# Kernel tuning notes

Hardware: AMD Instinct MI355X
Metric: run time of the kernel (lower is better)

## Reference

```python
import jax, jax.numpy as jnp
import numpy as np

N, M, K = 262144, 65536, 32
C_IN, C_OUT = 64, 128
BN_EPS = 1e-5


def setup_inputs() -> dict:
    key = jax.random.key(0)
    ks = jax.random.split(key, 6)
    p = jax.random.normal(ks[0], (N, 3), jnp.float32)
    x = jax.random.normal(ks[1], (N, C_IN), jnp.float32)
    o = jnp.array([N], jnp.int32)  # single-cloud batch offsets
    idx = jnp.sort(jax.random.randint(ks[2], (M,), 0, N))  # sampled point indices (FPS stand-in)
    knn_idx = jax.random.randint(ks[3], (M, K), 0, N)      # neighbor indices (ball-query/knn stand-in)
    # learned params: Linear(C_IN+3 -> C_OUT) + BatchNorm1d(C_OUT)
    W = jax.random.normal(ks[4], (C_IN + 3, C_OUT), jnp.float32) / np.sqrt(C_IN + 3).astype(np.float32)
    b = jnp.zeros((C_OUT,), jnp.float32)
    gamma = jnp.ones((C_OUT,), jnp.float32)
    beta = jnp.zeros((C_OUT,), jnp.float32)
    return dict(p=p, x=x, o=o, idx=idx, knn_idx=knn_idx, W=W, b=b, gamma=gamma, beta=beta)


def reference(p, x, o, idx, knn_idx, W, b, gamma, beta):
    # sampler: n_p = p[idx]
    n_p = p[idx]  # [M, 3]
    # pooling with with_xyz=True: gather K neighbors, concat relative xyz, max-pool over K
    rel = p[knn_idx] - n_p[:, None, :]                      # [M, K, 3]
    grouped = jnp.concatenate([rel, x[knn_idx]], axis=-1)   # [M, K, 3+C_IN]
    pooled = grouped.max(axis=1)                            # [M, 3+C_IN]
    # convs: Linear -> BatchNorm1d (training-mode batch stats) -> ReLU
    h = pooled @ W + b                                      # [M, C_OUT]
    mean = h.mean(axis=0)
    var = h.var(axis=0)
    h = (h - mean) * jax.lax.rsqrt(var + BN_EPS) * gamma + beta
    x_out = jnp.maximum(h, 0.0)
    n_o = jnp.array([idx.shape[0]], jnp.int32)
    return (n_p, x_out, n_o)
```

## Files before the change

kernel.cpp:

```cpp
#include <hip/hip_runtime.h>
#include <hip/hip_fp16.h>
#include <math.h>

#define K_NB   32
#define C_IN   64
#define C_OUT  128
#define KP     96
#define TILE   128
#define BN_EPS 1e-5f

typedef _Float16 f16x8 __attribute__((ext_vector_type(8)));
typedef float    f32x4 __attribute__((ext_vector_type(4)));
typedef float    f32x2 __attribute__((ext_vector_type(2)));

__device__ __forceinline__ unsigned pk(float a, float b) {
    __half2 h = __floats2half2_rn(a, b);
    return *reinterpret_cast<unsigned*>(&h);
}

__device__ __forceinline__ unsigned pkmax(unsigned a, unsigned b) {
    unsigned d;
    asm volatile("v_pk_max_f16 %0, %1, %2" : "=v"(d) : "v"(a), "v"(b));
    return d;
}

using pkrtz_t = decltype(__builtin_amdgcn_cvt_pkrtz(0.f, 0.f));
__device__ __forceinline__ unsigned h2u(pkrtz_t v) {
    union { pkrtz_t h; unsigned u; } c; c.h = v; return c.u;
}

__device__ __forceinline__ void fp8x4_to_h2x2(unsigned d, unsigned& lo, unsigned& hi) {
    f32x2 a = __builtin_amdgcn_cvt_pk_f32_fp8((int)d, false);
    f32x2 b = __builtin_amdgcn_cvt_pk_f32_fp8((int)d, true);
    lo = h2u(__builtin_amdgcn_cvt_pkrtz(a.x, a.y));
    hi = h2u(__builtin_amdgcn_cvt_pkrtz(b.x, b.y));
}

__global__ __launch_bounds__(256) void sa_zero(float* __restrict__ g, int n)
{
    for (int i = threadIdx.x; i < n; i += 256) g[i] = 0.f;
}

__global__ __launch_bounds__(256) void sa_cvt(
    const float4* __restrict__ x4, uint4* __restrict__ xq, int n16,
    float* __restrict__ gsum, int ng)
{
    if (blockIdx.x == 0)
        for (int i = threadIdx.x; i < ng; i += 256) gsum[i] = 0.f;
    for (int i = blockIdx.x * blockDim.x + threadIdx.x; i < n16;
         i += gridDim.x * blockDim.x) {
        float4 v0 = x4[4*i+0], v1 = x4[4*i+1], v2 = x4[4*i+2], v3 = x4[4*i+3];
        int w0 = 0, w1 = 0, w2 = 0, w3 = 0;
        w0 = __builtin_amdgcn_cvt_pk_fp8_f32(v0.x, v0.y, w0, false);
        w0 = __builtin_amdgcn_cvt_pk_fp8_f32(v0.z, v0.w, w0, true);
        w1 = __builtin_amdgcn_cvt_pk_fp8_f32(v1.x, v1.y, w1, false);
        w1 = __builtin_amdgcn_cvt_pk_fp8_f32(v1.z, v1.w, w1, true);
        w2 = __builtin_amdgcn_cvt_pk_fp8_f32(v2.x, v2.y, w2, false);
        w2 = __builtin_amdgcn_cvt_pk_fp8_f32(v2.z, v2.w, w2, true);
        w3 = __builtin_amdgcn_cvt_pk_fp8_f32(v3.x, v3.y, w3, false);
        w3 = __builtin_amdgcn_cvt_pk_fp8_f32(v3.z, v3.w, w3, true);
        xq[i] = make_uint4((unsigned)w0, (unsigned)w1, (unsigned)w2, (unsigned)w3);
    }
}

__global__ __launch_bounds__(256) void sa_pool_h(
    const float* __restrict__ p, const uint2* __restrict__ xq2,
    const int* __restrict__ idx, const int* __restrict__ knn,
    float* __restrict__ np_out, float* __restrict__ hbuf)
{
    const int lane = threadIdx.x & 63;
    const int wid  = threadIdx.x >> 6;
    const int m0   = blockIdx.x * 8 + wid * 2;
    const int half = lane >> 5;
    const int m    = m0 + half;

    const int kidx = knn[m0 * K_NB + lane];

    const int sub = lane & 7;
    const int g   = lane >> 3;
    uint2 u[8];
    #pragma unroll
    for (int i = 0; i < 4; ++i) {
        const int nbA = __shfl(kidx, i * 8 + g);
        u[i] = xq2[(size_t)nbA * 8 + sub];
    }
    #pragma unroll
    for (int i = 0; i < 4; ++i) {
        const int nbB = __shfl(kidx, 32 + i * 8 + g);
        u[4 + i] = xq2[(size_t)nbB * 8 + sub];
    }

    unsigned mx0 = 0xFC00FC00u, mx1 = 0xFC00FC00u, mx2 = 0xFC00FC00u, mx3 = 0xFC00FC00u;
    unsigned my0 = 0xFC00FC00u, my1 = 0xFC00FC00u, my2 = 0xFC00FC00u, my3 = 0xFC00FC00u;
    #pragma unroll
    for (int i = 0; i < 4; ++i) {
        unsigned h01, h23, h45, h67;
        fp8x4_to_h2x2(u[i].x, h01, h23);
        fp8x4_to_h2x2(u[i].y, h45, h67);
        mx0 = pkmax(mx0, h01); mx1 = pkmax(mx1, h23);
        mx2 = pkmax(mx2, h45); mx3 = pkmax(mx3, h67);
    }
    #pragma unroll
    for (int i = 0; i < 4; ++i) {
        unsigned h01, h23, h45, h67;
        fp8x4_to_h2x2(u[4 + i].x, h01, h23);
        fp8x4_to_h2x2(u[4 + i].y, h45, h67);
        my0 = pkmax(my0, h01); my1 = pkmax(my1, h23);
        my2 = pkmax(my2, h45); my3 = pkmax(my3, h67);
    }
    #pragma unroll
    for (int off = 8; off <= 32; off <<= 1) {
        mx0 = pkmax(mx0, (unsigned)__shfl_xor((int)mx0, off));
        mx1 = pkmax(mx1, (unsigned)__shfl_xor((int)mx1, off));
        mx2 = pkmax(mx2, (unsigned)__shfl_xor((int)mx2, off));
        mx3 = pkmax(mx3, (unsigned)__shfl_xor((int)mx3, off));
        my0 = pkmax(my0, (unsigned)__shfl_xor((int)my0, off));
        my1 = pkmax(my1, (unsigned)__shfl_xor((int)my1, off));
        my2 = pkmax(my2, (unsigned)__shfl_xor((int)my2, off));
        my3 = pkmax(my3, (unsigned)__shfl_xor((int)my3, off));
    }

    const float* pp = p + (size_t)kidx * 3;
    float px = pp[0], py = pp[1], pz = pp[2];
    #pragma unroll
    for (int off = 16; off >= 1; off >>= 1) {
        px = fmaxf(px, __shfl_xor(px, off));
        py = fmaxf(py, __shfl_xor(py, off));
        pz = fmaxf(pz, __shfl_xor(pz, off));
    }

    const int s = idx[m];
    const float npx = p[(size_t)s*3+0];
    const float npy = p[(size_t)s*3+1];
    const float npz = p[(size_t)s*3+2];
    if (lane < 3)                    np_out[(size_t)m0*3 + lane] = (lane == 0) ? npx : (lane == 1 ? npy : npz);
    else if (lane >= 32 && lane < 35) np_out[(size_t)(m0+1)*3 + (lane-32)] = (lane == 32) ? npx : (lane == 33 ? npy : npz);

    const float rx = px - npx, ry = py - npy, rz = pz - npz;

    const int t0 = m0 >> 7,       rl0 = m0 & (TILE - 1);
    const int t1 = (m0+1) >> 7,   rl1 = (m0+1) & (TILE - 1);
    __half* rowh0 = (__half*)(hbuf + (size_t)t0 * TILE * C_OUT) + rl0 * KP;
    __half* rowh1 = (__half*)(hbuf + (size_t)t1 * TILE * C_OUT) + rl1 * KP;

    if (lane < 8) {
        *(uint4*)(rowh0 + lane * 8) = make_uint4(mx0, mx1, mx2, mx3);
    } else if (lane < 16) {
        *(uint4*)(rowh1 + (lane - 8) * 8) = make_uint4(my0, my1, my2, my3);
    } else if (lane == 16) {
        *(uint4*)(rowh0 + 64) = make_uint4(pk(rx, ry), pk(rz, 0.f), 0u, 0u);
    } else if (lane >= 17 && lane < 20) {
        *(uint4*)(rowh0 + 64 + (lane - 16) * 8) = make_uint4(0u, 0u, 0u, 0u);
    } else if (lane == 48) {
        *(uint4*)(rowh1 + 64) = make_uint4(pk(rx, ry), pk(rz, 0.f), 0u, 0u);
    } else if (lane >= 49 && lane < 52) {
        *(uint4*)(rowh1 + 64 + (lane - 48) * 8) = make_uint4(0u, 0u, 0u, 0u);
    }
}

__global__ __launch_bounds__(256) void sa_pool_f(
    const float* __restrict__ p, const float* __restrict__ x,
    const int* __restrict__ idx, const int* __restrict__ knn,
    float* __restrict__ np_out, float* __restrict__ hbuf)
{
    const int lane = threadIdx.x & 63;
    const int m    = blockIdx.x * 4 + (threadIdx.x >> 6);
    int kidx = 0;
    if (lane < K_NB) kidx = knn[m * K_NB + lane];
    float xmax = -INFINITY;
    #pragma unroll
    for (int k = 0; k < K_NB; ++k) {
        int nb = __shfl(kidx, k);
        xmax = fmaxf(xmax, x[(size_t)nb * C_IN + lane]);
    }
    float px = -INFINITY, py = -INFINITY, pz = -INFINITY;
    if (lane < K_NB) {
        const float* pp = p + (size_t)kidx * 3;
        px = pp[0]; py = pp[1]; pz = pp[2];
    }
    #pragma unroll
    for (int off = 32; off >= 1; off >>= 1) {
        px = fmaxf(px, __shfl_xor(px, off));
        py = fmaxf(py, __shfl_xor(py, off));
        pz = fmaxf(pz, __shfl_xor(pz, off));
    }
    const int s = idx[m];
    const float npx = p[(size_t)s*3], npy = p[(size_t)s*3+1], npz = p[(size_t)s*3+2];
    if (lane < 3) np_out[(size_t)m*3 + lane] = (lane == 0) ? npx : (lane == 1 ? npy : npz);

    const int tile = m >> 7, rl = m & (TILE - 1);
    __half* rowh = (__half*)(hbuf + (size_t)tile * TILE * C_OUT) + rl * KP;
    if (lane < 8) {
        float v[8];
        #pragma unroll
        for (int j = 0; j < 8; ++j) v[j] = __shfl(xmax, lane * 8 + j);
        *(uint4*)(rowh + lane * 8) =
            make_uint4(pk(v[0],v[1]), pk(v[2],v[3]), pk(v[4],v[5]), pk(v[6],v[7]));
    } else if (lane == 8) {
        *(uint4*)(rowh + 64) = make_uint4(pk(px-npx, py-npy), pk(pz-npz, 0.f), 0u, 0u);
    } else if (lane < 12) {
        *(uint4*)(rowh + 64 + (lane - 8) * 8) = make_uint4(0u, 0u, 0u, 0u);
    }
}

__global__ __launch_bounds__(256) void sa_gemm_mfma(
    const float* __restrict__ W, const float* __restrict__ bias,
    float* __restrict__ h, float* __restrict__ gsum, unsigned rep_mask)
{
    __shared__ __half Wt[C_OUT][128];
    __shared__ float reds[16][C_OUT];
    __shared__ float redq[16][C_OUT];

    const int t    = threadIdx.x;
    const int wave = t >> 6, lane = t & 63;
    const int l15  = lane & 15, lg = lane >> 4;
    const int m0   = blockIdx.x * TILE;

    for (int e = t; e < C_OUT * KP; e += 256) {
        const int c = e & 127, kk = e >> 7;
        float w = 0.f;
        if (kk < C_IN)          w = W[(size_t)(3 + kk) * C_OUT + c];
        else if (kk < C_IN + 3) w = W[(size_t)(kk - C_IN) * C_OUT + c];
        Wt[c][(((kk >> 3) ^ (c & 7)) << 3) | (kk & 7)] = __float2half(w);
    }

    const __half* tb = (const __half*)(h + (size_t)blockIdx.x * TILE * C_OUT);
    f16x8 A[2][3];
    #pragma unroll
    for (int rt = 0; rt < 2; ++rt) {
        const int rl = wave * 32 + rt * 16 + l15;
        #pragma unroll
        for (int ks = 0; ks < 3; ++ks)
            A[rt][ks] = *(const f16x8*)(tb + (size_t)rl * KP + ks * 32 + lg * 8);
    }
    __syncthreads();

    f32x4 acc[2][8];
    #pragma unroll
    for (int ct = 0; ct < 8; ++ct) {
        const float bc = bias[ct * 16 + l15];
        acc[0][ct] = (f32x4){bc, bc, bc, bc};
        acc[1][ct] = (f32x4){bc, bc, bc, bc};
    }
    #pragma unroll
    for (int ks = 0; ks < 3; ++ks) {
        #pragma unroll
        for (int ct = 0; ct < 8; ++ct) {
            const int c  = ct * 16 + l15;
            const int kc = ks * 4 + lg;
            const f16x8 wf = *(const f16x8*)&Wt[c][((kc ^ (c & 7)) << 3)];
            acc[0][ct] = __builtin_amdgcn_mfma_f32_16x16x32_f16(A[0][ks], wf, acc[0][ct], 0, 0, 0);
            acc[1][ct] = __builtin_amdgcn_mfma_f32_16x16x32_f16(A[1][ks], wf, acc[1][ct], 0, 0, 0);
        }
    }

    float s8[8], q8[8];
    #pragma unroll
    for (int ct = 0; ct < 8; ++ct) { s8[ct] = 0.f; q8[ct] = 0.f; }
    #pragma unroll
    for (int rt = 0; rt < 2; ++rt) {
        #pragma unroll
        for (int ct = 0; ct < 8; ++ct) {
            const int col = ct * 16 + l15;
            #pragma unroll
            for (int r = 0; r < 4; ++r) {
                const int row = m0 + wave * 32 + rt * 16 + lg * 4 + r;
                const float v = acc[rt][ct][r];
                h[(size_t)row * C_OUT + col] = v;
                s8[ct] += v;
                q8[ct]  = fmaf(v, v, q8[ct]);
            }
        }
    }
    #pragma unroll
    for (int ct = 0; ct < 8; ++ct) {
        reds[wave * 4 + lg][ct * 16 + l15] = s8[ct];
        redq[wave * 4 + lg][ct * 16 + l15] = q8[ct];
    }
    __syncthreads();
    if (t < C_OUT) {
        float ss = 0.f, qq = 0.f;
        #pragma unroll
        for (int i = 0; i < 16; ++i) { ss += reds[i][t]; qq += redq[i][t]; }
        float* g = gsum + (size_t)(blockIdx.x & rep_mask) * 2 * C_OUT;
        atomicAdd(&g[t],         ss);
        atomicAdd(&g[C_OUT + t], qq);
    }
}

__global__ __launch_bounds__(256) void sa_bnrelu_fin(
    float* __restrict__ h, const float* __restrict__ gsum,
    const float* __restrict__ gamma, const float* __restrict__ beta,
    float* __restrict__ no_out, int M, int rep)
{
    __shared__ float sc[C_OUT], sh[C_OUT];
    const int t = threadIdx.x;
    if (t < C_OUT) {
        float s = 0.f, s2 = 0.f;
        for (int r = 0; r < rep; ++r) {
            s  += gsum[(size_t)r * 2 * C_OUT + t];
            s2 += gsum[(size_t)r * 2 * C_OUT + C_OUT + t];
        }
        const float inv_m = 1.0f / (float)M;
        const float mean = s * inv_m;
        const float var  = fmaf(-mean, mean, s2 * inv_m);
        const float scv  = gamma[t] * rsqrtf(var + BN_EPS);
        sc[t] = scv;
        sh[t] = fmaf(-mean, scv, beta[t]);
    }
    if (blockIdx.x == 0 && t == 0) no_out[0] = (float)M;
    __syncthreads();

    const size_t total4 = (size_t)M * C_OUT / 4;
    float4* h4 = (float4*)h;
    for (size_t i = (size_t)blockIdx.x * blockDim.x + t;
         i < total4; i += (size_t)gridDim.x * blockDim.x) {
        float4 v = h4[i];
        const int c = (int)((i * 4) & (C_OUT - 1));
        v.x = fmaxf(fmaf(v.x, sc[c+0], sh[c+0]), 0.f);
        v.y = fmaxf(fmaf(v.y, sc[c+1], sh[c+1]), 0.f);
        v.z = fmaxf(fmaf(v.z, sc[c+2], sh[c+2]), 0.f);
        v.w = fmaxf(fmaf(v.w, sc[c+3], sh[c+3]), 0.f);
        h4[i] = v;
    }
}

extern "C" void kernel_launch(void* const* d_in, const int* in_sizes, int n_in,
                              void* d_out, int out_size, void* d_ws, size_t ws_size,
                              hipStream_t stream)
{
    const float* p     = (const float*)d_in[0];
    const float* x     = (const float*)d_in[1];
    const int*   idx   = (const int*)d_in[3];
    const int*   knn   = (const int*)d_in[4];
    const float* W     = (const float*)d_in[5];
    const float* bias  = (const float*)d_in[6];
    const float* gamma = (const float*)d_in[7];
    const float* beta  = (const float*)d_in[8];

    const int N = in_sizes[1] / C_IN;
    const int M = in_sizes[3];

    float* out    = (float*)d_out;
    float* np_out = out;
    float* h      = out + (size_t)M * 3;
    float* no_out = out + (size_t)M * 3 + (size_t)M * C_OUT;

    const size_t xq_bytes = (size_t)N * C_IN;
    const bool   fp8_path = ws_size >= xq_bytes + 2048;

    const size_t tail = fp8_path ? (ws_size - xq_bytes) : ws_size;
    int rep = 1;
    while (rep < 8 && (size_t)(2 * rep) * 2 * C_OUT * sizeof(float) <= tail)
        rep <<= 1;

    float* gsum = fp8_path ? (float*)((char*)d_ws + xq_bytes) : (float*)d_ws;
    const unsigned rep_mask = (unsigned)(rep - 1);

    if (fp8_path) {
        uint4* xq = (uint4*)d_ws;
        const int n16 = N * C_IN / 16;
        sa_cvt   <<<2048, 256, 0, stream>>>((const float4*)x, xq, n16,
                                            gsum, rep * 2 * C_OUT);
        sa_pool_h<<<M / 8, 256, 0, stream>>>(p, (const uint2*)d_ws, idx, knn, np_out, h);
    } else {
        sa_zero  <<<1, 256, 0, stream>>>(gsum, rep * 2 * C_OUT);
        sa_pool_f<<<M / 4, 256, 0, stream>>>(p, x, idx, knn, np_out, h);
    }

    sa_gemm_mfma <<<M / TILE, 256, 0, stream>>>(W, bias, h, gsum, rep_mask);
    sa_bnrelu_fin<<<1024,     256, 0, stream>>>(h, gsum, gamma, beta, no_out, M, rep);
}
```

Baseline: 105.2 us.

## Store pre-BN activations as fp16 in the tile's upper half and retile BN kernel

The GEMM kernel now writes its pre-normalization outputs as fp16 into the second half of each tile's float region, not full fp32 rows, which halves that intermediate write and the later read. The BN/ReLU kernel is relaunched with one block per tile. Each block preloads its fp16 tile into registers before the barrier, then expands to fp32 and writes the final output over the same tile. Statistics are still accumulated in fp32, but the normalized values now carry fp16 rounding, and the in-place layout relies on each block reading its whole tile before writing.

```diff
diff --git a/kernel.cpp b/kernel.cpp
--- a/kernel.cpp
+++ b/kernel.cpp
@@ -16,6 +16,11 @@
 __device__ __forceinline__ unsigned pk(float a, float b) {
     __half2 h = __floats2half2_rn(a, b);
     return *reinterpret_cast<unsigned*>(&h);
+}
+
+__device__ __forceinline__ float2 uph(unsigned u) {
+    __half2 h = *reinterpret_cast<__half2*>(&u);
+    return __half22float2(h);
 }
 
 __device__ __forceinline__ unsigned pkmax(unsigned a, unsigned b) {
@@ -133,13 +138,13 @@
     const float npx = p[(size_t)s*3+0];
     const float npy = p[(size_t)s*3+1];
     const float npz = p[(size_t)s*3+2];
-    if (lane < 3)                    np_out[(size_t)m0*3 + lane] = (lane == 0) ? npx : (lane == 1 ? npy : npz);
+    if (lane < 3)                     np_out[(size_t)m0*3 + lane] = (lane == 0) ? npx : (lane == 1 ? npy : npz);
     else if (lane >= 32 && lane < 35) np_out[(size_t)(m0+1)*3 + (lane-32)] = (lane == 32) ? npx : (lane == 33 ? npy : npz);
 
     const float rx = px - npx, ry = py - npy, rz = pz - npz;
 
-    const int t0 = m0 >> 7,       rl0 = m0 & (TILE - 1);
-    const int t1 = (m0+1) >> 7,   rl1 = (m0+1) & (TILE - 1);
+    const int t0 = m0 >> 7,     rl0 = m0 & (TILE - 1);
+    const int t1 = (m0+1) >> 7, rl1 = (m0+1) & (TILE - 1);
     __half* rowh0 = (__half*)(hbuf + (size_t)t0 * TILE * C_OUT) + rl0 * KP;
     __half* rowh1 = (__half*)(hbuf + (size_t)t1 * TILE * C_OUT) + rl1 * KP;
 
@@ -214,7 +219,6 @@
     const int t    = threadIdx.x;
     const int wave = t >> 6, lane = t & 63;
     const int l15  = lane & 15, lg = lane >> 4;
-    const int m0   = blockIdx.x * TILE;
 
     for (int e = t; e < C_OUT * KP; e += 256) {
         const int c = e & 127, kk = e >> 7;
@@ -254,6 +258,7 @@
         }
     }
 
+    __half* outh = (__half*)(h + (size_t)blockIdx.x * TILE * C_OUT + 8192);
     float s8[8], q8[8];
     #pragma unroll
     for (int ct = 0; ct < 8; ++ct) { s8[ct] = 0.f; q8[ct] = 0.f; }
@@ -264,9 +269,9 @@
             const int col = ct * 16 + l15;
             #pragma unroll
             for (int r = 0; r < 4; ++r) {
-                const int row = m0 + wave * 32 + rt * 16 + lg * 4 + r;
+                const int rl = wave * 32 + rt * 16 + lg * 4 + r;
                 const float v = acc[rt][ct][r];
-                h[(size_t)row * C_OUT + col] = v;
+                outh[rl * C_OUT + col] = __float2half(v);
                 s8[ct] += v;
                 q8[ct]  = fmaf(v, v, q8[ct]);
             }
@@ -309,19 +314,36 @@
         sh[t] = fmaf(-mean, scv, beta[t]);
     }
     if (blockIdx.x == 0 && t == 0) no_out[0] = (float)M;
+
+    const size_t base = (size_t)blockIdx.x * TILE * C_OUT;
+    const uint4* src = (const uint4*)(h + base + 8192);
+    uint4 buf[8];
+    #pragma unroll
+    for (int i = 0; i < 8; ++i) buf[i] = src[i * 256 + t];
     __syncthreads();
 
-    const size_t total4 = (size_t)M * C_OUT / 4;
-    float4* h4 = (float4*)h;
-    for (size_t i = (size_t)blockIdx.x * blockDim.x + t;
-         i < total4; i += (size_t)gridDim.x * blockDim.x) {
-        float4 v = h4[i];
-        const int c = (int)((i * 4) & (C_OUT - 1));
-        v.x = fmaxf(fmaf(v.x, sc[c+0], sh[c+0]), 0.f);
-        v.y = fmaxf(fmaf(v.y, sc[c+1], sh[c+1]), 0.f);
-        v.z = fmaxf(fmaf(v.z, sc[c+2], sh[c+2]), 0.f);
-        v.w = fmaxf(fmaf(v.w, sc[c+3], sh[c+3]), 0.f);
-        h4[i] = v;
+    const int cbase = (t & 15) * 8;
+    float scr[8], shr[8];
+    #pragma unroll
+    for (int j = 0; j < 8; ++j) { scr[j] = sc[cbase + j]; shr[j] = sh[cbase + j]; }
+
+    float4* dst = (float4*)(h + base);
+    #pragma unroll
+    for (int i = 0; i < 8; ++i) {
+        const int ci = i * 256 + t;
+        float2 f0 = uph(buf[i].x), f1 = uph(buf[i].y);
+        float2 f2 = uph(buf[i].z), f3 = uph(buf[i].w);
+        float4 o0, o1;
+        o0.x = fmaxf(fmaf(f0.x, scr[0], shr[0]), 0.f);
+        o0.y = fmaxf(fmaf(f0.y, scr[1], shr[1]), 0.f);
+        o0.z = fmaxf(fmaf(f1.x, scr[2], shr[2]), 0.f);
+        o0.w = fmaxf(fmaf(f1.y, scr[3], shr[3]), 0.f);
+        o1.x = fmaxf(fmaf(f2.x, scr[4], shr[4]), 0.f);
+        o1.y = fmaxf(fmaf(f2.y, scr[5], shr[5]), 0.f);
+        o1.z = fmaxf(fmaf(f3.x, scr[6], shr[6]), 0.f);
+        o1.w = fmaxf(fmaf(f3.y, scr[7], shr[7]), 0.f);
+        dst[ci * 2 + 0] = o0;
+        dst[ci * 2 + 1] = o1;
     }
 }
 
@@ -369,5 +391,5 @@
     }
 
     sa_gemm_mfma <<<M / TILE, 256, 0, stream>>>(W, bias, h, gsum, rep_mask);
-    sa_bnrelu_fin<<<1024,     256, 0, stream>>>(h, gsum, gamma, beta, no_out, M, rep);
-}
+    sa_bnrelu_fin<<<M / TILE, 256, 0, stream>>>(h, gsum, gamma, beta, no_out, M, rep);
+}
```

Measured after the change: 105.9 us. About the same (+0.6%).
